# Kernel tuning notes

Hardware: AMD Instinct MI355X
Metric: run time of the kernel (lower is better)

## Reference

```python
import jax, jax.numpy as jnp
import numpy as np

DIM = 256
HEADS = 8
HEAD_DIM = DIM // HEADS  # 32
LN_EPS = 1e-5


def setup_inputs() -> dict:
    key = jax.random.key(0)
    ks = jax.random.split(key, 11)
    B, N = 8, 4096
    s = 1.0 / np.sqrt(DIM)
    return {
        "q": jax.random.normal(ks[0], (B, N, DIM), dtype=jnp.float32),
        "k": jax.random.normal(ks[1], (B, N, DIM), dtype=jnp.float32),
        "v": jax.random.normal(ks[2], (B, N, DIM), dtype=jnp.float32),
        "Wq": jax.random.normal(ks[3], (DIM, DIM), dtype=jnp.float32) * s,
        "bq": jax.random.normal(ks[4], (DIM,), dtype=jnp.float32) * 0.01,
        "Wk": jax.random.normal(ks[5], (DIM, DIM), dtype=jnp.float32) * s,
        "bk": jax.random.normal(ks[6], (DIM,), dtype=jnp.float32) * 0.01,
        "Wv": jax.random.normal(ks[7], (DIM, DIM), dtype=jnp.float32) * s,
        "bv": jax.random.normal(ks[8], (DIM,), dtype=jnp.float32) * 0.01,
        "ln_gamma": jnp.ones((DIM,), dtype=jnp.float32),
        "ln_beta": jnp.zeros((DIM,), dtype=jnp.float32),
    }


def _heads(x, B, N):
    # [B, N, DIM] -> [B, HEADS, N, HEAD_DIM]
    return x.reshape(B, N, HEADS, HEAD_DIM).transpose(0, 2, 1, 3)


def reference(q, k, v, Wq, bq, Wk, bk, Wv, bv, ln_gamma, ln_beta):
    B, N, _ = q.shape
    ql = _heads(q @ Wq.T + bq, B, N)
    kl = _heads(k @ Wk.T + bk, B, N)
    vl = _heads(v @ Wv.T + bv, B, N)

    # FFT-domain "attention": rfft2 over (seq, head_dim), complex multiply, irfft2
    q_fft = jnp.fft.rfft2(ql.astype(jnp.float32))   # [B, H, N, HEAD_DIM//2+1] complex
    k_fft = jnp.fft.rfft2(kl.astype(jnp.float32))
    attention = jnp.fft.irfft2(q_fft * k_fft)        # [B, H, N, HEAD_DIM]
    attention = jax.nn.softmax(attention, axis=-1)

    out = vl * attention                             # elementwise value gate
    out = out.transpose(0, 2, 1, 3).reshape(B, N, HEADS * HEAD_DIM)

    # dropout is identity at eval; residual + LayerNorm(256)
    out = out + v
    mu = jnp.mean(out, axis=-1, keepdims=True)
    var = jnp.var(out, axis=-1, keepdims=True)
    out = (out - mu) * jax.lax.rsqrt(var + LN_EPS) * ln_gamma + ln_beta
    return out
```

## Files before the change

kernel.cpp:

```cpp
#include <hip/hip_runtime.h>

#define NFREQ 2049

using cf = float2;
typedef __attribute__((ext_vector_type(8))) short short8;
typedef __attribute__((ext_vector_type(4))) float floatx4;

__device__ inline unsigned short bf16_rne(float x) {
  unsigned u = __float_as_uint(x);
  unsigned r = u + 0x7FFFu + ((u >> 16) & 1u);
  return (unsigned short)(r >> 16);
}
__device__ inline float bf16_to_f(unsigned short h) {
  return __uint_as_float(((unsigned)h) << 16);
}
__device__ inline unsigned pk_bf16(float a, float b) {
  unsigned r;
  asm("v_cvt_pk_bf16_f32 %0, %1, %2" : "=v"(r) : "v"(a), "v"(b));
  return r;
}
__device__ inline cf cmul(cf a, cf b) {
  return make_float2(a.x * b.x - a.y * b.y, a.x * b.y + a.y * b.x);
}
__device__ inline cf cadd(cf a, cf b) { return make_float2(a.x + b.x, a.y + b.y); }
__device__ inline cf csub(cf a, cf b) { return make_float2(a.x - b.x, a.y - b.y); }

__global__ __launch_bounds__(256) void wconv(
    const float* __restrict__ Wq, const float* __restrict__ Wk,
    const float* __restrict__ Wv,
    unsigned short* __restrict__ Whi, unsigned short* __restrict__ Wlo)
{
  int g = blockIdx.x * 256 + threadIdx.x;
  int c = g & 31, j = (g >> 5) & 255, z = g >> 13;
  const float* W = (z == 0) ? Wq : (z == 1) ? Wk : Wv;
  const float* s = W + (size_t)j * 256 + c * 8;
  float4 f0 = *(const float4*)s;
  float4 f1 = *(const float4*)(s + 4);
  unsigned h01 = pk_bf16(f0.x, f0.y), h23 = pk_bf16(f0.z, f0.w);
  unsigned h45 = pk_bf16(f1.x, f1.y), h67 = pk_bf16(f1.z, f1.w);
  float l0 = f0.x - __uint_as_float(h01 << 16);
  float l1 = f0.y - __uint_as_float(h01 & 0xFFFF0000u);
  float l2 = f0.z - __uint_as_float(h23 << 16);
  float l3 = f0.w - __uint_as_float(h23 & 0xFFFF0000u);
  float l4 = f1.x - __uint_as_float(h45 << 16);
  float l5 = f1.y - __uint_as_float(h45 & 0xFFFF0000u);
  float l6 = f1.z - __uint_as_float(h67 << 16);
  float l7 = f1.w - __uint_as_float(h67 & 0xFFFF0000u);
  size_t base = ((size_t)z * 8192 + c * 256 + j) * 8;
  *(uint4*)&Whi[base] = make_uint4(h01, h23, h45, h67);
  *(uint4*)&Wlo[base] = make_uint4(pk_bf16(l0, l1), pk_bf16(l2, l3),
                                   pk_bf16(l4, l5), pk_bf16(l6, l7));
}

__global__ __launch_bounds__(256, 4) void gemm_proj(
    const float* __restrict__ Xq, const float* __restrict__ bq,
    const float* __restrict__ Xk, const float* __restrict__ bk,
    const float* __restrict__ Xv, const float* __restrict__ bv,
    const unsigned short* __restrict__ Whi, const unsigned short* __restrict__ Wlo,
    float* __restrict__ dq, float* __restrict__ dk, float* __restrict__ dv)
{
  const int z = blockIdx.z;
  const float* X = (z == 0) ? Xq : (z == 1) ? Xk : Xv;
  const float* bias = (z == 0) ? bq : (z == 1) ? bk : bv;
  float* dst = (z == 0) ? dq : (z == 1) ? dk : dv;
  const unsigned short* WhiZ = Whi + (size_t)z * 65536;
  const unsigned short* WloZ = Wlo + (size_t)z * 65536;

  __shared__ __align__(16) unsigned short sm[2][8256];

  const int tid = threadIdx.x;
  const int m0 = blockIdx.x * 128;
  const int j0 = blockIdx.y * 64;
  const int wave = tid >> 6, lane = tid & 63;
  const int wm = wave & 1, wj = wave >> 1;
  const int lm = lane & 15, quad = lane >> 4;

  floatx4 acc[4][2] = {};

  int sIdx[2];
  const float* aSrc[2];
  #pragma unroll
  for (int r = 0; r < 2; r++) {
    int v = tid + r * 256;
    int row = v >> 2, q = v & 3;
    sIdx[r] = (q * 129 + row) << 3;
    aSrc[r] = X + (size_t)(m0 + row) * 256 + q * 8;
  }

  float4 xa[2][2];
  #pragma unroll
  for (int r = 0; r < 2; r++) {
    xa[r][0] = *(const float4*)(aSrc[r]);
    xa[r][1] = *(const float4*)(aSrc[r] + 4);
  }
  #pragma unroll
  for (int r = 0; r < 2; r++) {
    float4 f0 = xa[r][0], f1 = xa[r][1];
    unsigned h01 = pk_bf16(f0.x, f0.y), h23 = pk_bf16(f0.z, f0.w);
    unsigned h45 = pk_bf16(f1.x, f1.y), h67 = pk_bf16(f1.z, f1.w);
    float l0 = f0.x - __uint_as_float(h01 << 16);
    float l1 = f0.y - __uint_as_float(h01 & 0xFFFF0000u);
    float l2 = f0.z - __uint_as_float(h23 << 16);
    float l3 = f0.w - __uint_as_float(h23 & 0xFFFF0000u);
    float l4 = f1.x - __uint_as_float(h45 << 16);
    float l5 = f1.y - __uint_as_float(h45 & 0xFFFF0000u);
    float l6 = f1.z - __uint_as_float(h67 << 16);
    float l7 = f1.w - __uint_as_float(h67 & 0xFFFF0000u);
    *(uint4*)&sm[0][sIdx[r]] = make_uint4(h01, h23, h45, h67);
    *(uint4*)&sm[0][4128 + sIdx[r]] = make_uint4(pk_bf16(l0, l1), pk_bf16(l2, l3),
                                                 pk_bf16(l4, l5), pk_bf16(l6, l7));
  }
  #pragma unroll
  for (int r = 0; r < 2; r++) {
    xa[r][0] = *(const float4*)(aSrc[r] + 32);
    xa[r][1] = *(const float4*)(aSrc[r] + 36);
  }
  __syncthreads();

  for (int ks = 0; ks < 8; ks++) {
    const int p = ks & 1;

    short8 bhi[2], blo[2];
    #pragma unroll
    for (int jf = 0; jf < 2; jf++) {
      int c = ks * 4 + quad;
      int j = j0 + wj * 32 + jf * 16 + lm;
      size_t off = ((size_t)c * 256 + j) * 8;
      bhi[jf] = *(const short8*)&WhiZ[off];
      blo[jf] = *(const short8*)&WloZ[off];
    }

    short8 ahi[4], alo[4];
    #pragma unroll
    for (int mf = 0; mf < 4; mf++) {
      int row = wm * 64 + mf * 16 + lm;
      int idx = (quad * 129 + row) << 3;
      ahi[mf] = *(const short8*)&sm[p][idx];
      alo[mf] = *(const short8*)&sm[p][4128 + idx];
    }

    if (ks < 7) {
      #pragma unroll
      for (int r = 0; r < 2; r++) {
        float4 f0 = xa[r][0], f1 = xa[r][1];
        unsigned h01 = pk_bf16(f0.x, f0.y), h23 = pk_bf16(f0.z, f0.w);
        unsigned h45 = pk_bf16(f1.x, f1.y), h67 = pk_bf16(f1.z, f1.w);
        float l0 = f0.x - __uint_as_float(h01 << 16);
        float l1 = f0.y - __uint_as_float(h01 & 0xFFFF0000u);
        float l2 = f0.z - __uint_as_float(h23 << 16);
        float l3 = f0.w - __uint_as_float(h23 & 0xFFFF0000u);
        float l4 = f1.x - __uint_as_float(h45 << 16);
        float l5 = f1.y - __uint_as_float(h45 & 0xFFFF0000u);
        float l6 = f1.z - __uint_as_float(h67 << 16);
        float l7 = f1.w - __uint_as_float(h67 & 0xFFFF0000u);
        *(uint4*)&sm[p ^ 1][sIdx[r]] = make_uint4(h01, h23, h45, h67);
        *(uint4*)&sm[p ^ 1][4128 + sIdx[r]] =
            make_uint4(pk_bf16(l0, l1), pk_bf16(l2, l3),
                       pk_bf16(l4, l5), pk_bf16(l6, l7));
      }
      if (ks < 6) {
        #pragma unroll
        for (int r = 0; r < 2; r++) {
          const float* s = aSrc[r] + (ks + 2) * 32;
          xa[r][0] = *(const float4*)s;
          xa[r][1] = *(const float4*)(s + 4);
        }
      }
    }

    #pragma unroll
    for (int mf = 0; mf < 4; mf++)
      #pragma unroll
      for (int jf = 0; jf < 2; jf++) {
        acc[mf][jf] = __builtin_amdgcn_mfma_f32_16x16x32_bf16(
            ahi[mf], bhi[jf], acc[mf][jf], 0, 0, 0);
        acc[mf][jf] = __builtin_amdgcn_mfma_f32_16x16x32_bf16(
            ahi[mf], blo[jf], acc[mf][jf], 0, 0, 0);
        acc[mf][jf] = __builtin_amdgcn_mfma_f32_16x16x32_bf16(
            alo[mf], bhi[jf], acc[mf][jf], 0, 0, 0);
      }

    __syncthreads();
  }

  #pragma unroll
  for (int jf = 0; jf < 2; jf++) {
    float bj = bias[j0 + wj * 32 + jf * 16 + lm];
    #pragma unroll
    for (int mf = 0; mf < 4; mf++)
      #pragma unroll
      for (int r = 0; r < 4; r++)
        acc[mf][jf][r] += bj;
  }

  if (z == 2) {
    #pragma unroll
    for (int mf = 0; mf < 4; mf++)
      #pragma unroll
      for (int jf = 0; jf < 2; jf++) {
        int j = j0 + wj * 32 + jf * 16 + lm;
        int mb = m0 + wm * 64 + mf * 16 + quad * 4;
        #pragma unroll
        for (int r = 0; r < 4; r++)
          dst[(size_t)(mb + r) * 256 + j] = acc[mf][jf][r];
      }
  } else {
    const int b = m0 >> 12;
    const int n0 = m0 & 4095;
    #pragma unroll
    for (int mf = 0; mf < 4; mf++)
      #pragma unroll
      for (int jf = 0; jf < 2; jf++) {
        int j = j0 + wj * 32 + jf * 16 + lm;
        int nb = n0 + wm * 64 + mf * 16 + quad * 4;
        float4 o = make_float4(acc[mf][jf][0], acc[mf][jf][1],
                               acc[mf][jf][2], acc[mf][jf][3]);
        *(float4*)(dst + (size_t)(b * 256 + j) * 4096 + nb) = o;
      }
  }
}

#define FFT_LDS 4376

__device__ inline int swz(int i) { return i + (i >> 4) + (i >> 8) + (i >> 9); }
__device__ inline int digrev8(int n) {
  return ((n & 7) << 9) | (((n >> 3) & 7) << 6) | (((n >> 6) & 7) << 3) | ((n >> 9) & 7);
}

template<int SIGN>
__device__ inline void fft8_stages(cf* X, int tid)
{
  const float C = 0.70710678118654752f;
  const float sg = (float)SIGN;
  #pragma unroll
  for (int s = 0; s < 4; s++) {
    const int q = 1 << (3 * s);
    __syncthreads();
    #pragma unroll
    for (int r = 0; r < 2; r++) {
      int t = tid + r * 256;
      int j = t & (q - 1);
      int base = ((t >> (3 * s)) << (3 * s + 3)) + j;
      cf x[8];
      #pragma unroll
      for (int l = 0; l < 8; l++) x[l] = X[swz(base + l * q)];
      if (s > 0) {
        float a = sg * 6.283185307179586f * (float)j / (float)(8 * q);
        float sn, cs;
        __sincosf(a, &sn, &cs);
        cf w1 = make_float2(cs, sn);
        cf w = w1;
        #pragma unroll
        for (int l = 1; l < 8; l++) {
          x[l] = cmul(x[l], w);
          if (l < 7) w = cmul(w, w1);
        }
      }
      cf u0 = cadd(x[0], x[4]), v0 = csub(x[0], x[4]);
      cf u1 = cadd(x[1], x[5]), v1 = csub(x[1], x[5]);
      cf u2 = cadd(x[2], x[6]), v2 = csub(x[2], x[6]);
      cf u3 = cadd(x[3], x[7]), v3 = csub(x[3], x[7]);
      cf w1v = make_float2(C * (v1.x - sg * v1.y), C * (v1.y + sg * v1.x));
      cf w2v = make_float2(-sg * v2.y, sg * v2.x);
      cf w3v = make_float2(C * (-v3.x - sg * v3.y), C * (sg * v3.x - v3.y));
      cf e0 = cadd(u0, u2), e1 = csub(u0, u2);
      cf o0 = cadd(u1, u3), o1 = csub(u1, u3);
      cf F0 = cadd(e0, o0), F4 = csub(e0, o0);
      cf F2 = make_float2(e1.x - sg * o1.y, e1.y + sg * o1.x);
      cf F6 = make_float2(e1.x + sg * o1.y, e1.y - sg * o1.x);
      cf e0b = cadd(v0, w2v), e1b = csub(v0, w2v);
      cf o0b = cadd(w1v, w3v), o1b = csub(w1v, w3v);
      cf F1 = cadd(e0b, o0b), F5 = csub(e0b, o0b);
      cf F3 = make_float2(e1b.x - sg * o1b.y, e1b.y + sg * o1b.x);
      cf F7 = make_float2(e1b.x + sg * o1b.y, e1b.y - sg * o1b.x);
      X[swz(base + 0 * q)] = F0;
      X[swz(base + 1 * q)] = F1;
      X[swz(base + 2 * q)] = F2;
      X[swz(base + 3 * q)] = F3;
      X[swz(base + 4 * q)] = F4;
      X[swz(base + 5 * q)] = F5;
      X[swz(base + 6 * q)] = F6;
      X[swz(base + 7 * q)] = F7;
    }
  }
  __syncthreads();
}

__global__ __launch_bounds__(256) void fft_fwd(
    const float* __restrict__ srcQ, cf* __restrict__ dstQ,
    const float* __restrict__ srcK, cf* __restrict__ dstK)
{
  __shared__ cf X[FFT_LDS];
  const float* src_base = blockIdx.y ? srcK : srcQ;
  cf* dst_base = blockIdx.y ? dstK : dstQ;
  const int c0 = blockIdx.x * 2;
  const float* s0 = src_base + (size_t)c0 * 4096;
  const float* s1 = s0 + 4096;
  const int tid = threadIdx.x;
  #pragma unroll
  for (int i = 0; i < 16; i++) {
    int n = tid + i * 256;
    X[swz(digrev8(n))] = make_float2(s0[n], s1[n]);
  }
  fft8_stages<-1>(X, tid);
  cf* d0 = dst_base + (size_t)c0 * NFREQ;
  cf* d1 = d0 + NFREQ;
  for (int f = tid; f <= 2048; f += 256) {
    cf Zf = X[swz(f)];
    cf Zm = X[swz((4096 - f) & 4095)];
    d0[f] = make_float2(0.5f * (Zf.x + Zm.x), 0.5f * (Zf.y - Zm.y));
    d1[f] = make_float2(0.5f * (Zf.y + Zm.y), 0.5f * (Zm.x - Zf.x));
  }
}

__device__ inline cf tw_f(int l, int h) {
  int j = l & (h - 1);
  if (l & h) {
    float sn, cs;
    __sincosf(-3.14159265358979f * (float)j / (float)h, &sn, &cs);
    return make_float2(cs, sn);
  }
  return make_float2(1.0f, 0.0f);
}

template<int H>
__device__ inline cf fwd_stage(cf x, cf w, float sg) {
  float px = __shfl_xor(x.x, H);
  float py = __shfl_xor(x.y, H);
  return cmul(make_float2(px + sg * x.x, py + sg * x.y), w);
}
template<int H>
__device__ inline cf inv_stage(cf x, cf w, float sg) {
  cf t = cmul(x, w);
  float px = __shfl_xor(t.x, H);
  float py = __shfl_xor(t.y, H);
  return make_float2(px + sg * t.x, py + sg * t.y);
}
template<int H>
__device__ inline cf nt_stage(cf x, float sg) {
  float px = __shfl_xor(x.x, H);
  float py = __shfl_xor(x.y, H);
  return make_float2(px + sg * x.x, py + sg * x.y);
}

__global__ __launch_bounds__(256) void freq_conv(
    cf* __restrict__ Qf, const cf* __restrict__ Kf)
{
  __shared__ cf Qs[32][65];
  __shared__ cf Ks[32][65];
  const int f0 = blockIdx.x * 64;
  const int bh = blockIdx.y;
  const int tid = threadIdx.x;
  const int wave = tid >> 6, lane = tid & 63;
  const int d = lane & 31, hl = lane >> 5;

  #pragma unroll
  for (int i = 0; i < 8; i++) {
    int v = tid + i * 256;
    int e = v >> 6, fl = v & 63;
    int f = f0 + fl;
    if (f < NFREQ) {
      Qs[e][fl] = Qf[(size_t)(bh * 32 + e) * NFREQ + f];
      Ks[e][fl] = Kf[(size_t)(bh * 32 + e) * NFREQ + f];
    } else {
      Qs[e][fl] = make_float2(0.0f, 0.0f);
      Ks[e][fl] = make_float2(0.0f, 0.0f);
    }
  }
  __syncthreads();

  const cf w16 = tw_f(d, 16), w8 = tw_f(d, 8), w4 = tw_f(d, 4), w2 = tw_f(d, 2);
  const float s16 = (d & 16) ? -1.0f : 1.0f;
  const float s8  = (d & 8)  ? -1.0f : 1.0f;
  const float s4  = (d & 4)  ? -1.0f : 1.0f;
  const float s2  = (d & 2)  ? -1.0f : 1.0f;
  const float s1  = (d & 1)  ? -1.0f : 1.0f;

  #pragma unroll
  for (int it = 0; it < 8; it++) {
    const int fl = it * 8 + wave * 2 + hl;
    cf q = Qs[d][fl];
    cf k = Ks[d][fl];
    q = fwd_stage<16>(q, w16, s16);  k = fwd_stage<16>(k, w16, s16);
    q = fwd_stage<8>(q, w8, s8);     k = fwd_stage<8>(k, w8, s8);
    q = fwd_stage<4>(q, w4, s4);     k = fwd_stage<4>(k, w4, s4);
    q = fwd_stage<2>(q, w2, s2);     k = fwd_stage<2>(k, w2, s2);
    q = nt_stage<1>(q, s1);          k = nt_stage<1>(k, s1);
    cf c = cmul(q, k);
    c = nt_stage<1>(c, s1);
    c = inv_stage<2>(c, make_float2(w2.x, -w2.y), s2);
    c = inv_stage<4>(c, make_float2(w4.x, -w4.y), s4);
    c = inv_stage<8>(c, make_float2(w8.x, -w8.y), s8);
    c = inv_stage<16>(c, make_float2(w16.x, -w16.y), s16);
    Qs[d][fl] = make_float2(c.x * (1.0f / 32.0f), c.y * (1.0f / 32.0f));
  }
  __syncthreads();

  #pragma unroll
  for (int i = 0; i < 8; i++) {
    int v = tid + i * 256;
    int e = v >> 6, fl = v & 63;
    int f = f0 + fl;
    if (f < NFREQ)
      Qf[(size_t)(bh * 32 + e) * NFREQ + f] = Qs[e][fl];
  }
}

__global__ __launch_bounds__(256) void fft_inv(
    const cf* __restrict__ Cf, float* __restrict__ attn)
{
  __shared__ cf X[FFT_LDS];
  const int c0 = blockIdx.x * 2;
  const cf* s0 = Cf + (size_t)c0 * NFREQ;
  const cf* s1 = s0 + NFREQ;
  const int tid = threadIdx.x;
  for (int f = tid; f <= 2048; f += 256) {
    cf c1 = s0[f];
    cf c2 = s1[f];
    X[swz(digrev8(f))] = make_float2(c1.x - c2.y, c1.y + c2.x);
    if (f != 0 && f != 2048)
      X[swz(digrev8(4096 - f))] = make_float2(c1.x + c2.y, c2.x - c1.y);
  }
  fft8_stages<+1>(X, tid);
  float* d0 = attn + (size_t)c0 * 4096;
  float* d1 = d0 + 4096;
  const float inv = 1.0f / 4096.0f;
  #pragma unroll
  for (int i = 0; i < 16; i++) {
    int n = tid + i * 256;
    cf z = X[swz(n)];
    d0[n] = z.x * inv;
    d1[n] = z.y * inv;
  }
}

__global__ __launch_bounds__(256) void finalize_kernel(
    const float* __restrict__ attn, const float* __restrict__ VL,
    const float* __restrict__ vin, const float* __restrict__ gamma,
    const float* __restrict__ beta, float* __restrict__ out)
{
  __shared__ float At[256][33];
  const int n0 = blockIdx.x * 32;
  const int b = blockIdx.y;
  const int tid = threadIdx.x;
  #pragma unroll
  for (int i = 0; i < 32; i++) {
    int v = tid + i * 256;
    int hd = v >> 5, nn = v & 31;
    At[hd][nn] = attn[(size_t)(b * 256 + hd) * 4096 + n0 + nn];
  }
  __syncthreads();
  const int wave = tid >> 6, lane = tid & 63;
  float g[4], bt[4];
  #pragma unroll
  for (int r = 0; r < 4; r++) { g[r] = gamma[64 * r + lane]; bt[r] = beta[64 * r + lane]; }

  for (int t = 0; t < 8; t++) {
    const int nn = wave * 8 + t;
    const int n = n0 + nn;
    float p[4];
    #pragma unroll
    for (int r = 0; r < 4; r++) {
      float a = At[64 * r + lane][nn];
      float mx = a;
      #pragma unroll
      for (int off = 16; off >= 1; off >>= 1) mx = fmaxf(mx, __shfl_xor(mx, off, 32));
      float e = __expf(a - mx);
      float s = e;
      #pragma unroll
      for (int off = 16; off >= 1; off >>= 1) s += __shfl_xor(s, off, 32);
      p[r] = e / s;
    }
    const size_t base = ((size_t)b * 4096 + n) * 256 + lane;
    float o[4];
    float s1 = 0.0f, s2 = 0.0f;
    #pragma unroll
    for (int r = 0; r < 4; r++) {
      o[r] = VL[base + 64 * r] * p[r] + vin[base + 64 * r];
      s1 += o[r];
      s2 += o[r] * o[r];
    }
    #pragma unroll
    for (int off = 32; off >= 1; off >>= 1) {
      s1 += __shfl_xor(s1, off, 64);
      s2 += __shfl_xor(s2, off, 64);
    }
    float mu = s1 * (1.0f / 256.0f);
    float var = s2 * (1.0f / 256.0f) - mu * mu;
    float rs = rsqrtf(var + 1e-5f);
    #pragma unroll
    for (int r = 0; r < 4; r++)
      out[base + 64 * r] = (o[r] - mu) * rs * g[r] + bt[r];
  }
}

extern "C" void kernel_launch(void* const* d_in, const int* in_sizes, int n_in,
                              void* d_out, int out_size, void* d_ws, size_t ws_size,
                              hipStream_t stream)
{
  const float* q  = (const float*)d_in[0];
  const float* k  = (const float*)d_in[1];
  const float* v  = (const float*)d_in[2];
  const float* Wq = (const float*)d_in[3];
  const float* bq = (const float*)d_in[4];
  const float* Wk = (const float*)d_in[5];
  const float* bk = (const float*)d_in[6];
  const float* Wv = (const float*)d_in[7];
  const float* bv = (const float*)d_in[8];
  const float* ln_gamma = (const float*)d_in[9];
  const float* ln_beta  = (const float*)d_in[10];
  float* out = (float*)d_out;

  float* ws = (float*)d_ws;
  float* QL = ws;
  float* KL = QL + (size_t)8388608;
  float* VL = KL + (size_t)8388608;
  cf* Qf = (cf*)(VL + (size_t)8388608);
  cf* Kf = Qf + (size_t)2048 * NFREQ;
  float* attn = QL;

  unsigned short* Whi = (unsigned short*)Kf;
  unsigned short* Wlo = Whi + (size_t)3 * 65536;

  wconv<<<96, 256, 0, stream>>>(Wq, Wk, Wv, Whi, Wlo);

  gemm_proj<<<dim3(256, 4, 3), 256, 0, stream>>>(q, bq, k, bk, v, bv,
                                                 Whi, Wlo, QL, KL, VL);

  fft_fwd<<<dim3(1024, 2), 256, 0, stream>>>(QL, Qf, KL, Kf);

  freq_conv<<<dim3(33, 64), 256, 0, stream>>>(Qf, Kf);

  fft_inv<<<1024, 256, 0, stream>>>(Qf, attn);

  finalize_kernel<<<dim3(128, 8), 256, 0, stream>>>(attn, VL, v, ln_gamma,
                                                    ln_beta, out);
}
```

Before: 289.6 us.

## Retile projection GEMM to 64 rows by full 256 output columns per block

The projection GEMM block now covers 64 rows and all 256 output columns, with each wave owning 64 columns. Before, a block covered 128 rows by 64 columns, so each X row was loaded and split into bf16 hi/lo four times across the column blocks; now it is loaded and split once. The cost is twice the accumulators per thread, so launch bounds drop to 3 waves per SIMD, plus more B-fragment global loads per wave per k-step. A split8 helper is also factored out.

```diff
diff --git a/kernel.cpp b/kernel.cpp
--- a/kernel.cpp
+++ b/kernel.cpp
@@ -25,17 +25,7 @@
 __device__ inline cf cadd(cf a, cf b) { return make_float2(a.x + b.x, a.y + b.y); }
 __device__ inline cf csub(cf a, cf b) { return make_float2(a.x - b.x, a.y - b.y); }
 
-__global__ __launch_bounds__(256) void wconv(
-    const float* __restrict__ Wq, const float* __restrict__ Wk,
-    const float* __restrict__ Wv,
-    unsigned short* __restrict__ Whi, unsigned short* __restrict__ Wlo)
-{
-  int g = blockIdx.x * 256 + threadIdx.x;
-  int c = g & 31, j = (g >> 5) & 255, z = g >> 13;
-  const float* W = (z == 0) ? Wq : (z == 1) ? Wk : Wv;
-  const float* s = W + (size_t)j * 256 + c * 8;
-  float4 f0 = *(const float4*)s;
-  float4 f1 = *(const float4*)(s + 4);
+__device__ inline void split8(float4 f0, float4 f1, uint4* hi, uint4* lo) {
   unsigned h01 = pk_bf16(f0.x, f0.y), h23 = pk_bf16(f0.z, f0.w);
   unsigned h45 = pk_bf16(f1.x, f1.y), h67 = pk_bf16(f1.z, f1.w);
   float l0 = f0.x - __uint_as_float(h01 << 16);
@@ -46,13 +36,28 @@
   float l5 = f1.y - __uint_as_float(h45 & 0xFFFF0000u);
   float l6 = f1.z - __uint_as_float(h67 << 16);
   float l7 = f1.w - __uint_as_float(h67 & 0xFFFF0000u);
+  *hi = make_uint4(h01, h23, h45, h67);
+  *lo = make_uint4(pk_bf16(l0, l1), pk_bf16(l2, l3),
+                   pk_bf16(l4, l5), pk_bf16(l6, l7));
+}
+
+__global__ __launch_bounds__(256) void wconv(
+    const float* __restrict__ Wq, const float* __restrict__ Wk,
+    const float* __restrict__ Wv,
+    unsigned short* __restrict__ Whi, unsigned short* __restrict__ Wlo)
+{
+  int g = blockIdx.x * 256 + threadIdx.x;
+  int c = g & 31, j = (g >> 5) & 255, z = g >> 13;
+  const float* W = (z == 0) ? Wq : (z == 1) ? Wk : Wv;
+  const float* s = W + (size_t)j * 256 + c * 8;
+  uint4 hi, lo;
+  split8(*(const float4*)s, *(const float4*)(s + 4), &hi, &lo);
   size_t base = ((size_t)z * 8192 + c * 256 + j) * 8;
-  *(uint4*)&Whi[base] = make_uint4(h01, h23, h45, h67);
-  *(uint4*)&Wlo[base] = make_uint4(pk_bf16(l0, l1), pk_bf16(l2, l3),
-                                   pk_bf16(l4, l5), pk_bf16(l6, l7));
-}
-
-__global__ __launch_bounds__(256, 4) void gemm_proj(
+  *(uint4*)&Whi[base] = hi;
+  *(uint4*)&Wlo[base] = lo;
+}
+
+__global__ __launch_bounds__(256, 3) void gemm_proj(
     const float* __restrict__ Xq, const float* __restrict__ bq,
     const float* __restrict__ Xk, const float* __restrict__ bk,
     const float* __restrict__ Xv, const float* __restrict__ bv,
@@ -66,66 +71,43 @@
   const unsigned short* WhiZ = Whi + (size_t)z * 65536;
   const unsigned short* WloZ = Wlo + (size_t)z * 65536;
 
-  __shared__ __align__(16) unsigned short sm[2][8256];
+  __shared__ __align__(16) unsigned short sm[2][4160];
 
   const int tid = threadIdx.x;
-  const int m0 = blockIdx.x * 128;
-  const int j0 = blockIdx.y * 64;
+  const int m0 = blockIdx.x * 64;
   const int wave = tid >> 6, lane = tid & 63;
-  const int wm = wave & 1, wj = wave >> 1;
   const int lm = lane & 15, quad = lane >> 4;
 
-  floatx4 acc[4][2] = {};
-
-  int sIdx[2];
-  const float* aSrc[2];
-  #pragma unroll
-  for (int r = 0; r < 2; r++) {
-    int v = tid + r * 256;
-    int row = v >> 2, q = v & 3;
-    sIdx[r] = (q * 129 + row) << 3;
-    aSrc[r] = X + (size_t)(m0 + row) * 256 + q * 8;
-  }
-
-  float4 xa[2][2];
-  #pragma unroll
-  for (int r = 0; r < 2; r++) {
-    xa[r][0] = *(const float4*)(aSrc[r]);
-    xa[r][1] = *(const float4*)(aSrc[r] + 4);
-  }
-  #pragma unroll
-  for (int r = 0; r < 2; r++) {
-    float4 f0 = xa[r][0], f1 = xa[r][1];
-    unsigned h01 = pk_bf16(f0.x, f0.y), h23 = pk_bf16(f0.z, f0.w);
-    unsigned h45 = pk_bf16(f1.x, f1.y), h67 = pk_bf16(f1.z, f1.w);
-    float l0 = f0.x - __uint_as_float(h01 << 16);
-    float l1 = f0.y - __uint_as_float(h01 & 0xFFFF0000u);
-    float l2 = f0.z - __uint_as_float(h23 << 16);
-    float l3 = f0.w - __uint_as_float(h23 & 0xFFFF0000u);
-    float l4 = f1.x - __uint_as_float(h45 << 16);
-    float l5 = f1.y - __uint_as_float(h45 & 0xFFFF0000u);
-    float l6 = f1.z - __uint_as_float(h67 << 16);
-    float l7 = f1.w - __uint_as_float(h67 & 0xFFFF0000u);
-    *(uint4*)&sm[0][sIdx[r]] = make_uint4(h01, h23, h45, h67);
-    *(uint4*)&sm[0][4128 + sIdx[r]] = make_uint4(pk_bf16(l0, l1), pk_bf16(l2, l3),
-                                                 pk_bf16(l4, l5), pk_bf16(l6, l7));
-  }
-  #pragma unroll
-  for (int r = 0; r < 2; r++) {
-    xa[r][0] = *(const float4*)(aSrc[r] + 32);
-    xa[r][1] = *(const float4*)(aSrc[r] + 36);
-  }
+  floatx4 acc[4][4] = {};
+
+  const int srow = tid >> 2, sq = tid & 3;
+  const int sIdx = (sq * 65 + srow) << 3;
+  const float* aSrc = X + (size_t)(m0 + srow) * 256 + sq * 8;
+
+  int bOff[4];
+  #pragma unroll
+  for (int jf = 0; jf < 4; jf++) {
+    int j = wave * 64 + jf * 16 + lm;
+    bOff[jf] = ((quad * 256) + j) << 3;
+  }
+
+  {
+    uint4 hi, lo;
+    split8(*(const float4*)(aSrc), *(const float4*)(aSrc + 4), &hi, &lo);
+    *(uint4*)&sm[0][sIdx] = hi;
+    *(uint4*)&sm[0][2080 + sIdx] = lo;
+  }
+  float4 xa0 = *(const float4*)(aSrc + 32);
+  float4 xa1 = *(const float4*)(aSrc + 36);
   __syncthreads();
 
   for (int ks = 0; ks < 8; ks++) {
     const int p = ks & 1;
 
-    short8 bhi[2], blo[2];
-    #pragma unroll
-    for (int jf = 0; jf < 2; jf++) {
-      int c = ks * 4 + quad;
-      int j = j0 + wj * 32 + jf * 16 + lm;
-      size_t off = ((size_t)c * 256 + j) * 8;
+    short8 bhi[4], blo[4];
+    #pragma unroll
+    for (int jf = 0; jf < 4; jf++) {
+      int off = bOff[jf] + ks * 8192;
       bhi[jf] = *(const short8*)&WhiZ[off];
       blo[jf] = *(const short8*)&WloZ[off];
     }
@@ -133,45 +115,27 @@
     short8 ahi[4], alo[4];
     #pragma unroll
     for (int mf = 0; mf < 4; mf++) {
-      int row = wm * 64 + mf * 16 + lm;
-      int idx = (quad * 129 + row) << 3;
+      int idx = (quad * 65 + mf * 16 + lm) << 3;
       ahi[mf] = *(const short8*)&sm[p][idx];
-      alo[mf] = *(const short8*)&sm[p][4128 + idx];
+      alo[mf] = *(const short8*)&sm[p][2080 + idx];
     }
 
     if (ks < 7) {
-      #pragma unroll
-      for (int r = 0; r < 2; r++) {
-        float4 f0 = xa[r][0], f1 = xa[r][1];
-        unsigned h01 = pk_bf16(f0.x, f0.y), h23 = pk_bf16(f0.z, f0.w);
-        unsigned h45 = pk_bf16(f1.x, f1.y), h67 = pk_bf16(f1.z, f1.w);
-        float l0 = f0.x - __uint_as_float(h01 << 16);
-        float l1 = f0.y - __uint_as_float(h01 & 0xFFFF0000u);
-        float l2 = f0.z - __uint_as_float(h23 << 16);
-        float l3 = f0.w - __uint_as_float(h23 & 0xFFFF0000u);
-        float l4 = f1.x - __uint_as_float(h45 << 16);
-        float l5 = f1.y - __uint_as_float(h45 & 0xFFFF0000u);
-        float l6 = f1.z - __uint_as_float(h67 << 16);
-        float l7 = f1.w - __uint_as_float(h67 & 0xFFFF0000u);
-        *(uint4*)&sm[p ^ 1][sIdx[r]] = make_uint4(h01, h23, h45, h67);
-        *(uint4*)&sm[p ^ 1][4128 + sIdx[r]] =
-            make_uint4(pk_bf16(l0, l1), pk_bf16(l2, l3),
-                       pk_bf16(l4, l5), pk_bf16(l6, l7));
+      uint4 hi, lo;
+      split8(xa0, xa1, &hi, &lo);
+      *(uint4*)&sm[p ^ 1][sIdx] = hi;
+      *(uint4*)&sm[p ^ 1][2080 + sIdx] = lo;
+      if (ks < 6) {
+        const float* s = aSrc + (ks + 2) * 32;
+        xa0 = *(const float4*)s;
+        xa1 = *(const float4*)(s + 4);
       }
-      if (ks < 6) {
-        #pragma unroll
-        for (int r = 0; r < 2; r++) {
-          const float* s = aSrc[r] + (ks + 2) * 32;
-          xa[r][0] = *(const float4*)s;
-          xa[r][1] = *(const float4*)(s + 4);
-        }
-      }
     }
 
     #pragma unroll
     for (int mf = 0; mf < 4; mf++)
       #pragma unroll
-      for (int jf = 0; jf < 2; jf++) {
+      for (int jf = 0; jf < 4; jf++) {
         acc[mf][jf] = __builtin_amdgcn_mfma_f32_16x16x32_bf16(
             ahi[mf], bhi[jf], acc[mf][jf], 0, 0, 0);
         acc[mf][jf] = __builtin_amdgcn_mfma_f32_16x16x32_bf16(
@@ -184,8 +148,8 @@
   }
 
   #pragma unroll
-  for (int jf = 0; jf < 2; jf++) {
-    float bj = bias[j0 + wj * 32 + jf * 16 + lm];
+  for (int jf = 0; jf < 4; jf++) {
+    float bj = bias[wave * 64 + jf * 16 + lm];
     #pragma unroll
     for (int mf = 0; mf < 4; mf++)
       #pragma unroll
@@ -197,9 +161,9 @@
     #pragma unroll
     for (int mf = 0; mf < 4; mf++)
       #pragma unroll
-      for (int jf = 0; jf < 2; jf++) {
-        int j = j0 + wj * 32 + jf * 16 + lm;
-        int mb = m0 + wm * 64 + mf * 16 + quad * 4;
+      for (int jf = 0; jf < 4; jf++) {
+        int j = wave * 64 + jf * 16 + lm;
+        int mb = m0 + mf * 16 + quad * 4;
         #pragma unroll
         for (int r = 0; r < 4; r++)
           dst[(size_t)(mb + r) * 256 + j] = acc[mf][jf][r];
@@ -210,9 +174,9 @@
     #pragma unroll
     for (int mf = 0; mf < 4; mf++)
       #pragma unroll
-      for (int jf = 0; jf < 2; jf++) {
-        int j = j0 + wj * 32 + jf * 16 + lm;
-        int nb = n0 + wm * 64 + mf * 16 + quad * 4;
+      for (int jf = 0; jf < 4; jf++) {
+        int j = wave * 64 + jf * 16 + lm;
+        int nb = n0 + mf * 16 + quad * 4;
         float4 o = make_float4(acc[mf][jf][0], acc[mf][jf][1],
                                acc[mf][jf][2], acc[mf][jf][3]);
         *(float4*)(dst + (size_t)(b * 256 + j) * 4096 + nb) = o;
@@ -524,7 +488,7 @@
 
   wconv<<<96, 256, 0, stream>>>(Wq, Wk, Wv, Whi, Wlo);
 
-  gemm_proj<<<dim3(256, 4, 3), 256, 0, stream>>>(q, bq, k, bk, v, bv,
+  gemm_proj<<<dim3(512, 1, 3), 256, 0, stream>>>(q, bq, k, bk, v, bv,
                                                  Whi, Wlo, QL, KL, VL);
 
   fft_fwd<<<dim3(1024, 2), 256, 0, stream>>>(QL, Qf, KL, Kf);
```

New measurement: 289.9 us. About the same (+0.1%).
